# Kernel tuning notes

Measured on AMD Instinct MI355X. Metric: run time of the kernel, lower is better.

Reference implementation:

```python
import jax, jax.numpy as jnp
import numpy as np

HEADS = 16
EPS = 1e-5

def _ln(x, g, b):
    m = jnp.mean(x, axis=-1, keepdims=True)
    v = jnp.mean((x - m) ** 2, axis=-1, keepdims=True)
    return (x - m) * jax.lax.rsqrt(v + EPS) * g + b

def setup_inputs() -> dict:
    key = jax.random.key(0)
    ks = jax.random.split(key, 12)
    B, N, C, H = 4, 2048, 1024, 4096
    d = {}
    d['x'] = jax.random.normal(ks[0], (B, N, C), jnp.float32)
    d['pos_embed'] = jax.random.normal(ks[1], (1, N, C), jnp.float32)
    # LayerNorm params (normq, normk, normv, norm)
    for nm in ['nq', 'nk', 'nv', 'n']:
        d[nm + '_g'] = jnp.ones((C,), jnp.float32)
        d[nm + '_b'] = jnp.zeros((C,), jnp.float32)
    s = 1.0 / np.sqrt(C)
    d['wq'] = jax.random.uniform(ks[2], (C, C), jnp.float32, -s, s)
    d['bq'] = jnp.zeros((C,), jnp.float32)
    d['wk'] = jax.random.uniform(ks[3], (C, C), jnp.float32, -s, s)
    d['bk'] = jnp.zeros((C,), jnp.float32)
    d['wv'] = jax.random.uniform(ks[4], (C, C), jnp.float32, -s, s)
    d['bv'] = jnp.zeros((C,), jnp.float32)
    d['wp'] = jax.random.uniform(ks[5], (C, C), jnp.float32, -s, s)
    d['bp'] = jnp.zeros((C,), jnp.float32)
    d['w1'] = jax.random.uniform(ks[6], (C, H), jnp.float32, -s, s)
    d['b1'] = jnp.zeros((H,), jnp.float32)
    sh = 1.0 / np.sqrt(H)
    d['w2'] = jax.random.uniform(ks[7], (H, C), jnp.float32, -sh, sh)
    d['b2'] = jnp.zeros((C,), jnp.float32)
    return d

def reference(x, pos_embed, nq_g, nq_b, nk_g, nk_b, nv_g, nv_b, wq, bq, wk, bk, wv, bv, wp, bp, n_g, n_b, w1, b1, w2, b2):
    B, N, C = x.shape
    hd = C // HEADS
    scale = hd ** -0.5
    q_in = x
    k_in = x + pos_embed
    v_in = x + pos_embed
    # Attention (eval mode: dropout = identity)
    q = (_ln(q_in, nq_g, nq_b) @ wq + bq).reshape(B, N, HEADS, hd)
    k = (_ln(k_in, nk_g, nk_b) @ wk + bk).reshape(B, N, HEADS, hd)
    v = (_ln(v_in, nv_g, nv_b) @ wv + bv).reshape(B, N, HEADS, hd)
    attn = jnp.einsum('bqhd,bkhd->bhqk', q, k) * scale
    attn = jax.nn.softmax(attn, axis=-1)
    out = jnp.einsum('bhqk,bkhd->bqhd', attn, v).reshape(B, N, C)
    out = out @ wp + bp
    # residual + MLP
    h = q_in + out
    y = _ln(h, n_g, n_b) @ w1 + b1
    y = jnp.where(y >= 0, y, 0.1 * y)  # LeakyReLU(0.1)
    y = y @ w2 + b2
    return h + y
```

## Files before the change

### kernel.cpp

```cpp
#include <hip/hip_runtime.h>
#include <hip/hip_bf16.h>

#define DEV __device__ __forceinline__

typedef __attribute__((ext_vector_type(8))) short short8;
typedef __attribute__((ext_vector_type(4))) short short4v;
typedef __attribute__((ext_vector_type(4))) float f32x4;
typedef __attribute__((ext_vector_type(2))) int int2v;

constexpr int Bb   = 4;
constexpr int SEQ  = 2048;
constexpr int C    = 1024;
constexpr int HID  = 4096;
constexpr int NH   = 16;
constexpr int HD   = 64;
constexpr int MTOT = Bb * SEQ;

DEV unsigned bfbits(float f) {
  unsigned x = __float_as_uint(f);
  return (x + 0x7fffu + ((x >> 16) & 1u)) >> 16;
}

DEV short f2bf(float f) { return (short)bfbits(f); }

DEV unsigned packrn(float a, float b) {
  unsigned ua = __float_as_uint(a) + 0x8000u;
  unsigned ub = __float_as_uint(b) + 0x8000u;
  return __builtin_amdgcn_perm(ub, ua, 0x07060302u);
}

DEV float fexp2(float x) {
#if __has_builtin(__builtin_amdgcn_exp2f)
  return __builtin_amdgcn_exp2f(x);
#else
  float r;
  asm("v_exp_f32 %0, %1" : "=v"(r) : "v"(x));
  return r;
#endif
}

DEV void gload16(const void* g, void* l) {
  __builtin_amdgcn_global_load_lds((const __attribute__((address_space(1))) void*)g,
                                   (__attribute__((address_space(3))) void*)l, 16, 0, 0);
}

DEV f32x4 mfma16(short4v a, short4v b, f32x4 c) {
#if __has_builtin(__builtin_amdgcn_mfma_f32_16x16x16bf16_1k)
  return __builtin_amdgcn_mfma_f32_16x16x16bf16_1k(a, b, c, 0, 0, 0);
#else
  asm volatile("v_mfma_f32_16x16x16_bf16 %0, %1, %2, %0" : "+v"(c) : "v"(a), "v"(b));
  return c;
#endif
}

DEV void transpose_body(const float* __restrict__ src, short* __restrict__ dst,
                        int R, int Cc) {
  __shared__ float t[32][33];
  int tx = threadIdx.x & 31, ty = threadIdx.x >> 5;
  int c0 = blockIdx.x * 32, r0 = blockIdx.y * 32;
  #pragma unroll
  for (int i = 0; i < 4; i++)
    t[ty + i * 8][tx] = src[(size_t)(r0 + ty + i * 8) * Cc + c0 + tx];
  __syncthreads();
  #pragma unroll
  for (int i = 0; i < 4; i++)
    dst[(size_t)(c0 + ty + i * 8) * R + r0 + tx] = f2bf(t[tx][ty + i * 8]);
}

__global__ void k_transpose_w(const float* __restrict__ src, short* __restrict__ dst,
                              int R, int Cc) {
  transpose_body(src, dst, R, Cc);
}

__global__ void k_transpose_w4(const float* __restrict__ s0, const float* __restrict__ s1,
                               const float* __restrict__ s2, const float* __restrict__ s3,
                               short* __restrict__ d0, short* __restrict__ d1,
                               short* __restrict__ d2, short* __restrict__ d3) {
  const float* s = blockIdx.z == 0 ? s0 : blockIdx.z == 1 ? s1 : blockIdx.z == 2 ? s2 : s3;
  short*       d = blockIdx.z == 0 ? d0 : blockIdx.z == 1 ? d1 : blockIdx.z == 2 ? d2 : d3;
  transpose_body(s, d, C, C);
}

__global__ void k_transpose_v(const short* __restrict__ V, short* __restrict__ Vt) {
  __shared__ short t[32][33];
  int tx = threadIdx.x & 31, ty = threadIdx.x >> 5;
  int plane = blockIdx.z;
  int b = plane >> 4, h = plane & 15;
  int n0 = blockIdx.x * 32, d0 = blockIdx.y * 32;
  #pragma unroll
  for (int i = 0; i < 4; i++)
    t[ty + i * 8][tx] = V[(size_t)(b * SEQ + n0 + ty + i * 8) * C + h * HD + d0 + tx];
  __syncthreads();
  #pragma unroll
  for (int i = 0; i < 4; i++)
    Vt[((size_t)plane * HD + d0 + ty + i * 8) * SEQ + n0 + tx] = t[tx][ty + i * 8];
}

__global__ void k_ln_qkv(const float* __restrict__ x, const float* __restrict__ pos,
                         const float* __restrict__ nqg, const float* __restrict__ nqb,
                         const float* __restrict__ nkg, const float* __restrict__ nkb,
                         const float* __restrict__ nvg, const float* __restrict__ nvb,
                         short* __restrict__ xq, short* __restrict__ xk,
                         short* __restrict__ xv) {
  int row = blockIdx.x, tid = threadIdx.x;
  int n = row & (SEQ - 1);
  float a4[4], p4[4];
  float s1 = 0, s2 = 0, t1 = 0, t2 = 0;
  #pragma unroll
  for (int i = 0; i < 4; i++) {
    int c = tid + i * 256;
    float a = x[(size_t)row * C + c];
    float p = pos[(size_t)n * C + c] + a;
    a4[i] = a; p4[i] = p;
    s1 += a; s2 += a * a; t1 += p; t2 += p * p;
  }
  #pragma unroll
  for (int off = 32; off; off >>= 1) {
    s1 += __shfl_xor(s1, off, 64);
    s2 += __shfl_xor(s2, off, 64);
    t1 += __shfl_xor(t1, off, 64);
    t2 += __shfl_xor(t2, off, 64);
  }
  __shared__ float red[4][4];
  int wave = tid >> 6, lane = tid & 63;
  if (lane == 0) { red[wave][0] = s1; red[wave][1] = s2; red[wave][2] = t1; red[wave][3] = t2; }
  __syncthreads();
  s1 = red[0][0] + red[1][0] + red[2][0] + red[3][0];
  s2 = red[0][1] + red[1][1] + red[2][1] + red[3][1];
  t1 = red[0][2] + red[1][2] + red[2][2] + red[3][2];
  t2 = red[0][3] + red[1][3] + red[2][3] + red[3][3];
  float mq = s1 * (1.f / C), mk = t1 * (1.f / C);
  float rq = rsqrtf(s2 * (1.f / C) - mq * mq + 1e-5f);
  float rk = rsqrtf(t2 * (1.f / C) - mk * mk + 1e-5f);
  #pragma unroll
  for (int i = 0; i < 4; i++) {
    int c = tid + i * 256;
    float nq_ = (a4[i] - mq) * rq;
    float nk_ = (p4[i] - mk) * rk;
    xq[(size_t)row * C + c] = f2bf(nq_ * nqg[c] + nqb[c]);
    xk[(size_t)row * C + c] = f2bf(nk_ * nkg[c] + nkb[c]);
    xv[(size_t)row * C + c] = f2bf(nk_ * nvg[c] + nvb[c]);
  }
}

__global__ void k_ln1(const float* __restrict__ h, const float* __restrict__ g,
                      const float* __restrict__ bta, short* __restrict__ out) {
  int row = blockIdx.x, tid = threadIdx.x;
  float a4[4];
  float s1 = 0, s2 = 0;
  #pragma unroll
  for (int i = 0; i < 4; i++) {
    int c = tid + i * 256;
    float a = h[(size_t)row * C + c];
    a4[i] = a; s1 += a; s2 += a * a;
  }
  #pragma unroll
  for (int off = 32; off; off >>= 1) {
    s1 += __shfl_xor(s1, off, 64);
    s2 += __shfl_xor(s2, off, 64);
  }
  __shared__ float red[4][2];
  int wave = tid >> 6, lane = tid & 63;
  if (lane == 0) { red[wave][0] = s1; red[wave][1] = s2; }
  __syncthreads();
  s1 = red[0][0] + red[1][0] + red[2][0] + red[3][0];
  s2 = red[0][1] + red[1][1] + red[2][1] + red[3][1];
  float m = s1 * (1.f / C);
  float r = rsqrtf(s2 * (1.f / C) - m * m + 1e-5f);
  #pragma unroll
  for (int i = 0; i < 4; i++) {
    int c = tid + i * 256;
    out[(size_t)row * C + c] = f2bf((a4[i] - m) * r * g[c] + bta[c]);
  }
}

template <int MODE>
DEV void gemm8_body(const short* __restrict__ A, const short* __restrict__ Bt,
                    const float* __restrict__ bias, const float* __restrict__ resid,
                    void* __restrict__ outp, int Nn, int Kk, float scale,
                    int m0, int n0, short* __restrict__ sA, short* __restrict__ sB) {
  constexpr int AO = 128 * 64, BO = 256 * 64;
  const int tid = threadIdx.x;
  const int wave = tid >> 6, lane = tid & 63, quad = lane >> 4, l15 = lane & 15;
  const int wm = (wave >> 2) * 64, wn = (wave & 3) * 64;

  const int sr = tid >> 3, su = tid & 7;
  const int sx = (su ^ (sr & 7)) * 8;
  const short* gA0 = A + (size_t)(m0 + sr) * Kk + sx;
  const short* gA1 = gA0 + (size_t)64 * Kk;
  const short* gB0 = Bt + (size_t)(n0 + sr) * Kk + sx;
  const short* gB1 = gB0 + (size_t)64 * Kk;
  const short* gB2 = gB0 + (size_t)128 * Kk;
  const short* gB3 = gB0 + (size_t)192 * Kk;

  const f32x4 fzero = {0.f, 0.f, 0.f, 0.f};
  f32x4 acc[4][4];
  #pragma unroll
  for (int mi = 0; mi < 4; mi++)
    #pragma unroll
    for (int ni = 0; ni < 4; ni++) acc[mi][ni] = fzero;

  const int nkt = Kk >> 6;

  auto stg = [&](int t) {
    const int b_ = t % 3, ko = t << 6;
    gload16(gA0 + ko, &sA[(size_t)b_ * AO + (size_t)tid * 8]);
    gload16(gA1 + ko, &sA[(size_t)b_ * AO + (size_t)(512 + tid) * 8]);
    gload16(gB0 + ko, &sB[(size_t)b_ * BO + (size_t)tid * 8]);
    gload16(gB1 + ko, &sB[(size_t)b_ * BO + (size_t)(512 + tid) * 8]);
    gload16(gB2 + ko, &sB[(size_t)b_ * BO + (size_t)(1024 + tid) * 8]);
    gload16(gB3 + ko, &sB[(size_t)b_ * BO + (size_t)(1536 + tid) * 8]);
  };
  auto stgA_ = [&](int t) {
    const int b_ = t % 3, ko = t << 6;
    gload16(gA0 + ko, &sA[(size_t)b_ * AO + (size_t)tid * 8]);
    gload16(gA1 + ko, &sA[(size_t)b_ * AO + (size_t)(512 + tid) * 8]);
    gload16(gB0 + ko, &sB[(size_t)b_ * BO + (size_t)tid * 8]);
  };
  auto stgB_ = [&](int t) {
    const int b_ = t % 3, ko = t << 6;
    gload16(gB1 + ko, &sB[(size_t)b_ * BO + (size_t)(512 + tid) * 8]);
    gload16(gB2 + ko, &sB[(size_t)b_ * BO + (size_t)(1024 + tid) * 8]);
    gload16(gB3 + ko, &sB[(size_t)b_ * BO + (size_t)(1536 + tid) * 8]);
  };

  stg(0);
  if (nkt > 1) stg(1);

  for (int t = 0; t < nkt; t++) {
    if (t + 1 < nkt) asm volatile("s_waitcnt vmcnt(6)" ::: "memory");
    else             asm volatile("s_waitcnt vmcnt(0)" ::: "memory");
    __builtin_amdgcn_s_barrier();
    const short* a_ = &sA[(size_t)(t % 3) * AO];
    const short* b_ = &sB[(size_t)(t % 3) * BO];
    short8 av[4][2];
    {
      short8 bv[2][2];
      #pragma unroll
      for (int m2 = 0; m2 < 4; m2++) {
        const int rA = wm + m2 * 16 + l15, sw = rA & 7;
        #pragma unroll
        for (int ks = 0; ks < 2; ks++)
          av[m2][ks] = *(const short8*)&a_[rA * 64 + ((ks * 4 + quad) ^ sw) * 8];
      }
      #pragma unroll
      for (int n2 = 0; n2 < 2; n2++) {
        const int rB = wn + n2 * 16 + l15, sw = rB & 7;
        #pragma unroll
        for (int ks = 0; ks < 2; ks++)
          bv[n2][ks] = *(const short8*)&b_[rB * 64 + ((ks * 4 + quad) ^ sw) * 8];
      }
      if (t + 2 < nkt) stgA_(t + 2);
      __builtin_amdgcn_s_barrier();
      asm volatile("s_waitcnt lgkmcnt(0)" ::: "memory");
      __builtin_amdgcn_sched_barrier(0);
      __builtin_amdgcn_s_setprio(1);
      #pragma unroll
      for (int ks = 0; ks < 2; ks++)
        #pragma unroll
        for (int m2 = 0; m2 < 4; m2++)
          #pragma unroll
          for (int n2 = 0; n2 < 2; n2++)
            acc[m2][n2] = __builtin_amdgcn_mfma_f32_16x16x32_bf16(
                av[m2][ks], bv[n2][ks], acc[m2][n2], 0, 0, 0);
      __builtin_amdgcn_s_setprio(0);
      __builtin_amdgcn_s_barrier();
    }
    {
      short8 bv[2][2];
      #pragma unroll
      for (int n2 = 0; n2 < 2; n2++) {
        const int rB = wn + (2 + n2) * 16 + l15, sw = rB & 7;
        #pragma unroll
        for (int ks = 0; ks < 2; ks++)
          bv[n2][ks] = *(const short8*)&b_[rB * 64 + ((ks * 4 + quad) ^ sw) * 8];
      }
      if (t + 2 < nkt) stgB_(t + 2);
      __builtin_amdgcn_s_barrier();
      asm volatile("s_waitcnt lgkmcnt(0)" ::: "memory");
      __builtin_amdgcn_sched_barrier(0);
      __builtin_amdgcn_s_setprio(1);
      #pragma unroll
      for (int ks = 0; ks < 2; ks++)
        #pragma unroll
        for (int m2 = 0; m2 < 4; m2++)
          #pragma unroll
          for (int n2 = 0; n2 < 2; n2++)
            acc[m2][2 + n2] = __builtin_amdgcn_mfma_f32_16x16x32_bf16(
                av[m2][ks], bv[n2][ks], acc[m2][2 + n2], 0, 0, 0);
      __builtin_amdgcn_s_setprio(0);
      __builtin_amdgcn_s_barrier();
    }
  }

  float bb[4];
  #pragma unroll
  for (int ni = 0; ni < 4; ni++) bb[ni] = bias[n0 + wn + ni * 16 + l15];
  #pragma unroll
  for (int mi = 0; mi < 4; mi++) {
    #pragma unroll
    for (int ni = 0; ni < 4; ni++) {
      #pragma unroll
      for (int r = 0; r < 4; r++) {
        int row = m0 + wm + mi * 16 + quad * 4 + r;
        int col = n0 + wn + ni * 16 + l15;
        float v = (acc[mi][ni][r] + bb[ni]) * scale;
        if constexpr (MODE == 1) v = v >= 0.f ? v : 0.1f * v;
        if constexpr (MODE == 2)
          ((float*)outp)[(size_t)row * Nn + col] = resid[(size_t)row * Nn + col] + v;
        else
          ((short*)outp)[(size_t)row * Nn + col] = f2bf(v);
      }
    }
  }
}

template <int MODE>
__global__ __launch_bounds__(512, 1)
void k_gemm8(const short* __restrict__ A, const short* __restrict__ Bt,
             const float* __restrict__ bias, const float* __restrict__ resid,
             void* __restrict__ outp, int Nn, int Kk) {
  __shared__ __align__(16) short sA[3 * 128 * 64];
  __shared__ __align__(16) short sB[3 * 256 * 64];
  gemm8_body<MODE>(A, Bt, bias, resid, outp, Nn, Kk, 1.0f,
                   blockIdx.x * 128, blockIdx.y * 256, sA, sB);
}

__global__ __launch_bounds__(512, 1)
void k_gemm8_qkv(const short* __restrict__ xq, const short* __restrict__ xk,
                 const short* __restrict__ xv,
                 const short* __restrict__ wqT, const short* __restrict__ wkT,
                 const short* __restrict__ wvT,
                 const float* __restrict__ bq, const float* __restrict__ bk,
                 const float* __restrict__ bv,
                 short* __restrict__ Qm, short* __restrict__ Km, short* __restrict__ Vm) {
  __shared__ __align__(16) short sA[3 * 128 * 64];
  __shared__ __align__(16) short sB[3 * 256 * 64];
  const int z = blockIdx.z;
  const short* A    = z == 0 ? xq : z == 1 ? xk : xv;
  const short* Bt   = z == 0 ? wqT : z == 1 ? wkT : wvT;
  const float* bias = z == 0 ? bq : z == 1 ? bk : bv;
  short* outp       = z == 0 ? Qm : z == 1 ? Km : Vm;
  const float scale = z == 0 ? 0.1803368801111244f : 1.0f;
  gemm8_body<0>(A, Bt, bias, nullptr, outp, C, C, scale,
                blockIdx.x * 128, blockIdx.y * 256, sA, sB);
}

__global__ __launch_bounds__(256, 4)
void k_attn(const short* __restrict__ Q, const short* __restrict__ K,
            const short* __restrict__ Vt, short* __restrict__ O) {
  __shared__ __align__(16) short sK[2][64 * 64];
  __shared__ __align__(16) short sV[2][64 * 64];
  const int tid = threadIdx.x;
  const int bh = blockIdx.x;
  const int b = bh >> 4, h = bh & 15;
  const int q0 = blockIdx.y * 128;
  const int wave = tid >> 6, lane = tid & 63, quad = lane >> 4, l15 = lane & 15;
  const int wm = wave * 32;
  const size_t tokBase = (size_t)b * SEQ;

  short8 qf[2][2];
  #pragma unroll
  for (int qi = 0; qi < 2; qi++)
    #pragma unroll
    for (int hf = 0; hf < 2; hf++)
      qf[qi][hf] = *(const short8*)(Q + (tokBase + q0 + wm + qi * 16 + l15) * C
                                    + h * HD + hf * 32 + quad * 8);

  const int r0 = tid >> 3,        c0s = ((tid & 7) ^ (r0 & 7)) * 8;
  const int r1 = (tid + 256) >> 3, c1s = ((tid & 7) ^ (r1 & 7)) * 8;
  const short* gK0 = K + (tokBase + r0) * C + h * HD + c0s;
  const short* gK1 = K + (tokBase + r1) * C + h * HD + c1s;
  const short* gV0 = Vt + ((size_t)bh * HD + r0) * SEQ + c0s;
  const short* gV1 = Vt + ((size_t)bh * HD + r1) * SEQ + c1s;
  short* lK0 = &sK[0][tid * 8];
  short* lK1 = &sK[0][(tid + 256) * 8];
  short* lV0 = &sV[0][tid * 8];
  short* lV1 = &sV[0][(tid + 256) * 8];
  constexpr int BUFO = 64 * 64;

#define STAGE(bufsel, kb) {                                   \
    int kk = (kb) * 64, bo = (bufsel) * BUFO;                 \
    gload16(gK0 + (size_t)kk * C, lK0 + bo);                  \
    gload16(gK1 + (size_t)kk * C, lK1 + bo);                  \
    gload16(gV0 + kk,             lV0 + bo);                  \
    gload16(gV1 + kk,             lV1 + bo); }

  const f32x4 fzero = {0.f, 0.f, 0.f, 0.f};
  const short4v onesv = {0x3F80, 0x3F80, 0x3F80, 0x3F80};
  f32x4 o[2][4];
  f32x4 oSum[2] = {fzero, fzero};
  #pragma unroll
  for (int qi = 0; qi < 2; qi++)
    #pragma unroll
    for (int di = 0; di < 4; di++) o[qi][di] = fzero;

  const int sw = l15 & 7;

  STAGE(0, 0)

  for (int kb = 0; kb < SEQ / 64; kb++) {
    const int buf = kb & 1;
    __syncthreads();
    if (kb + 1 < SEQ / 64) STAGE(buf ^ 1, kb + 1)

    unsigned pk[4][2][2];
    #pragma unroll
    for (int ki = 0; ki < 4; ki++) {
      const int krow = (ki * 16 + l15) * 64;
      short8 a0 = *(const short8*)&sK[buf][krow + ((0 + quad) ^ sw) * 8];
      short8 a1 = *(const short8*)&sK[buf][krow + ((4 + quad) ^ sw) * 8];
      #pragma unroll
      for (int qi = 0; qi < 2; qi++) {
        f32x4 st = __builtin_amdgcn_mfma_f32_16x16x32_bf16(a0, qf[qi][0], fzero, 0, 0, 0);
        st = __builtin_amdgcn_mfma_f32_16x16x32_bf16(a1, qf[qi][1], st, 0, 0, 0);
        float p0 = fexp2(st[0]), p1 = fexp2(st[1]);
        float p2 = fexp2(st[2]), p3 = fexp2(st[3]);
        pk[ki][qi][0] = packrn(p0, p1);
        pk[ki][qi][1] = packrn(p2, p3);
      }
    }

    #pragma unroll
    for (int ki = 0; ki < 4; ki++) {
      short4v bv[4];
      const int g = ((ki * 2 + (quad >> 1)) ^ sw) * 8 + (quad & 1) * 4;
      #pragma unroll
      for (int di = 0; di < 4; di++)
        bv[di] = *(const short4v*)&sV[buf][(di * 16 + l15) * 64 + g];
      #pragma unroll
      for (int qi = 0; qi < 2; qi++) {
        int2v t; t.x = (int)pk[ki][qi][0]; t.y = (int)pk[ki][qi][1];
        short4v aP = __builtin_bit_cast(short4v, t);
        oSum[qi] = mfma16(aP, onesv, oSum[qi]);
        #pragma unroll
        for (int di = 0; di < 4; di++)
          o[qi][di] = mfma16(aP, bv[di], o[qi][di]);
      }
    }
  }
#undef STAGE

  float linv[2][4];
  #pragma unroll
  for (int qi = 0; qi < 2; qi++)
    #pragma unroll
    for (int r = 0; r < 4; r++)
      linv[qi][r] = 1.0f / oSum[qi][r];

  #pragma unroll
  for (int qi = 0; qi < 2; qi++)
    #pragma unroll
    for (int di = 0; di < 4; di++)
      #pragma unroll
      for (int r = 0; r < 4; r++) {
        int row = q0 + wm + qi * 16 + quad * 4 + r;
        int col = h * HD + di * 16 + l15;
        O[(tokBase + row) * C + col] = f2bf(o[qi][di][r] * linv[qi][r]);
      }
}

extern "C" void kernel_launch(void* const* d_in, const int* in_sizes, int n_in,
                              void* d_out, int out_size, void* d_ws, size_t ws_size,
                              hipStream_t stream) {
  const float* x   = (const float*)d_in[0];
  const float* pos = (const float*)d_in[1];
  const float* nqg = (const float*)d_in[2];
  const float* nqb = (const float*)d_in[3];
  const float* nkg = (const float*)d_in[4];
  const float* nkb = (const float*)d_in[5];
  const float* nvg = (const float*)d_in[6];
  const float* nvb = (const float*)d_in[7];
  const float* ng  = (const float*)d_in[8];
  const float* nb  = (const float*)d_in[9];
  const float* wq  = (const float*)d_in[10];
  const float* bq  = (const float*)d_in[11];
  const float* wk  = (const float*)d_in[12];
  const float* bk  = (const float*)d_in[13];
  const float* wv  = (const float*)d_in[14];
  const float* bv  = (const float*)d_in[15];
  const float* wp  = (const float*)d_in[16];
  const float* bp  = (const float*)d_in[17];
  const float* w1  = (const float*)d_in[18];
  const float* b1  = (const float*)d_in[19];
  const float* w2  = (const float*)d_in[20];
  const float* b2  = (const float*)d_in[21];

  char* ws = (char*)d_ws;
  const size_t MB = 1u << 20;
  short* wqT  = (short*)(ws + 0 * MB);
  short* wkT  = (short*)(ws + 2 * MB);
  short* wvT  = (short*)(ws + 4 * MB);
  short* wpT  = (short*)(ws + 6 * MB);
  short* w1T  = (short*)(ws + 8 * MB);
  short* w2T  = (short*)(ws + 16 * MB);
  short* xq   = (short*)(ws + 24 * MB);
  short* xk   = (short*)(ws + 40 * MB);
  short* xv   = (short*)(ws + 56 * MB);
  short* Qm   = (short*)(ws + 72 * MB);
  short* Km   = (short*)(ws + 88 * MB);
  short* Vm   = (short*)(ws + 104 * MB);
  short* Vt   = (short*)(ws + 120 * MB);
  short* y1   = (short*)(ws + 72 * MB);
  short* Ob   = xk;
  short* hln  = xq;
  float* hbuf = (float*)(ws + 136 * MB);
  (void)ws_size; (void)in_sizes; (void)n_in; (void)out_size;

  dim3 blk(256);
  k_transpose_w4<<<dim3(32, 32, 4), blk, 0, stream>>>(wq, wk, wv, wp, wqT, wkT, wvT, wpT);
  k_transpose_w<<<dim3(128, 32), blk, 0, stream>>>(w1, w1T, C, HID);
  k_transpose_w<<<dim3(32, 128), blk, 0, stream>>>(w2, w2T, HID, C);
  k_ln_qkv<<<dim3(MTOT), blk, 0, stream>>>(x, pos, nqg, nqb, nkg, nkb, nvg, nvb, xq, xk, xv);
  k_gemm8_qkv<<<dim3(MTOT / 128, C / 256, 3), dim3(512), 0, stream>>>(
      xq, xk, xv, wqT, wkT, wvT, bq, bk, bv, Qm, Km, Vm);
  k_transpose_v<<<dim3(SEQ / 32, HD / 32, Bb * NH), blk, 0, stream>>>(Vm, Vt);
  k_attn<<<dim3(Bb * NH, SEQ / 128), blk, 0, stream>>>(Qm, Km, Vt, Ob);
  k_gemm8<2><<<dim3(MTOT / 128, C / 256), dim3(512), 0, stream>>>(Ob, wpT, bp, x, hbuf, C, C);
  k_ln1<<<dim3(MTOT), blk, 0, stream>>>(hbuf, ng, nb, hln);
  k_gemm8<1><<<dim3(MTOT / 128, HID / 256), dim3(512), 0, stream>>>(hln, w1T, b1, nullptr,
                                                                    y1, HID, C);
  k_gemm8<2><<<dim3(MTOT / 128, C / 256), dim3(512), 0, stream>>>(y1, w2T, b2, hbuf,
                                                                  (float*)d_out, C, HID);
}
```

Before: 524.9 us.

## Enlarge GEMM tiles to 256x256 with double-buffered four-phase staging

```diff
diff --git a/kernel.cpp b/kernel.cpp
--- a/kernel.cpp
+++ b/kernel.cpp
@@ -175,82 +175,66 @@
 }
 
 template <int MODE>
-DEV void gemm8_body(const short* __restrict__ A, const short* __restrict__ Bt,
+DEV void gemm2_body(const short* __restrict__ A, const short* __restrict__ Bt,
                     const float* __restrict__ bias, const float* __restrict__ resid,
                     void* __restrict__ outp, int Nn, int Kk, float scale,
                     int m0, int n0, short* __restrict__ sA, short* __restrict__ sB) {
-  constexpr int AO = 128 * 64, BO = 256 * 64;
+  constexpr int TO = 256 * 64;
   const int tid = threadIdx.x;
   const int wave = tid >> 6, lane = tid & 63, quad = lane >> 4, l15 = lane & 15;
-  const int wm = (wave >> 2) * 64, wn = (wave & 3) * 64;
+  const int wm = (wave >> 2) * 128, wn = (wave & 3) * 64;
 
   const int sr = tid >> 3, su = tid & 7;
   const int sx = (su ^ (sr & 7)) * 8;
   const short* gA0 = A + (size_t)(m0 + sr) * Kk + sx;
-  const short* gA1 = gA0 + (size_t)64 * Kk;
   const short* gB0 = Bt + (size_t)(n0 + sr) * Kk + sx;
-  const short* gB1 = gB0 + (size_t)64 * Kk;
-  const short* gB2 = gB0 + (size_t)128 * Kk;
-  const short* gB3 = gB0 + (size_t)192 * Kk;
 
   const f32x4 fzero = {0.f, 0.f, 0.f, 0.f};
-  f32x4 acc[4][4];
-  #pragma unroll
-  for (int mi = 0; mi < 4; mi++)
+  f32x4 acc[8][4];
+  #pragma unroll
+  for (int mi = 0; mi < 8; mi++)
     #pragma unroll
     for (int ni = 0; ni < 4; ni++) acc[mi][ni] = fzero;
 
   const int nkt = Kk >> 6;
 
-  auto stg = [&](int t) {
-    const int b_ = t % 3, ko = t << 6;
-    gload16(gA0 + ko, &sA[(size_t)b_ * AO + (size_t)tid * 8]);
-    gload16(gA1 + ko, &sA[(size_t)b_ * AO + (size_t)(512 + tid) * 8]);
-    gload16(gB0 + ko, &sB[(size_t)b_ * BO + (size_t)tid * 8]);
-    gload16(gB1 + ko, &sB[(size_t)b_ * BO + (size_t)(512 + tid) * 8]);
-    gload16(gB2 + ko, &sB[(size_t)b_ * BO + (size_t)(1024 + tid) * 8]);
-    gload16(gB3 + ko, &sB[(size_t)b_ * BO + (size_t)(1536 + tid) * 8]);
+  auto stgPair = [&](int t, int p) {
+    const int b_ = t & 1, ko = t << 6;
+    gload16(gA0 + (size_t)(p * 64) * Kk + ko,
+            &sA[(size_t)b_ * TO + (size_t)p * 4096 + (size_t)tid * 8]);
+    gload16(gB0 + (size_t)(p * 64) * Kk + ko,
+            &sB[(size_t)b_ * TO + (size_t)p * 4096 + (size_t)tid * 8]);
   };
-  auto stgA_ = [&](int t) {
-    const int b_ = t % 3, ko = t << 6;
-    gload16(gA0 + ko, &sA[(size_t)b_ * AO + (size_t)tid * 8]);
-    gload16(gA1 + ko, &sA[(size_t)b_ * AO + (size_t)(512 + tid) * 8]);
-    gload16(gB0 + ko, &sB[(size_t)b_ * BO + (size_t)tid * 8]);
-  };
-  auto stgB_ = [&](int t) {
-    const int b_ = t % 3, ko = t << 6;
-    gload16(gB1 + ko, &sB[(size_t)b_ * BO + (size_t)(512 + tid) * 8]);
-    gload16(gB2 + ko, &sB[(size_t)b_ * BO + (size_t)(1024 + tid) * 8]);
-    gload16(gB3 + ko, &sB[(size_t)b_ * BO + (size_t)(1536 + tid) * 8]);
-  };
-
-  stg(0);
-  if (nkt > 1) stg(1);
+
+  #pragma unroll
+  for (int p = 0; p < 4; p++) stgPair(0, p);
 
   for (int t = 0; t < nkt; t++) {
-    if (t + 1 < nkt) asm volatile("s_waitcnt vmcnt(6)" ::: "memory");
-    else             asm volatile("s_waitcnt vmcnt(0)" ::: "memory");
+    asm volatile("s_waitcnt vmcnt(0)" ::: "memory");
     __builtin_amdgcn_s_barrier();
-    const short* a_ = &sA[(size_t)(t % 3) * AO];
-    const short* b_ = &sB[(size_t)(t % 3) * BO];
-    short8 av[4][2];
-    {
-      short8 bv[2][2];
-      #pragma unroll
-      for (int m2 = 0; m2 < 4; m2++) {
-        const int rA = wm + m2 * 16 + l15, sw = rA & 7;
+    const short* a_ = &sA[(size_t)(t & 1) * TO];
+    const short* b_ = &sB[(size_t)(t & 1) * TO];
+    short8 bv[4][2];
+    #pragma unroll
+    for (int ph = 0; ph < 4; ph++) {
+      short8 av[2][2];
+      #pragma unroll
+      for (int m2 = 0; m2 < 2; m2++) {
+        const int rA = wm + (ph * 2 + m2) * 16 + l15, sw = rA & 7;
         #pragma unroll
         for (int ks = 0; ks < 2; ks++)
           av[m2][ks] = *(const short8*)&a_[rA * 64 + ((ks * 4 + quad) ^ sw) * 8];
       }
-      #pragma unroll
-      for (int n2 = 0; n2 < 2; n2++) {
-        const int rB = wn + n2 * 16 + l15, sw = rB & 7;
+      if (ph == 0) {
         #pragma unroll
-        for (int ks = 0; ks < 2; ks++)
-          bv[n2][ks] = *(const short8*)&b_[rB * 64 + ((ks * 4 + quad) ^ sw) * 8];
-      }
-      if (t + 2 < nkt) stgA_(t + 2);
+        for (int n2 = 0; n2 < 4; n2++) {
+          const int rB = wn + n2 * 16 + l15, sw = rB & 7;
+          #pragma unroll
+          for (int ks = 0; ks < 2; ks++)
+            bv[n2][ks] = *(const short8*)&b_[rB * 64 + ((ks * 4 + quad) ^ sw) * 8];
+        }
+      }
+      if (t + 1 < nkt) stgPair(t + 1, ph);
       __builtin_amdgcn_s_barrier();
       asm volatile("s_waitcnt lgkmcnt(0)" ::: "memory");
       __builtin_amdgcn_sched_barrier(0);
@@ -258,46 +242,21 @@
       #pragma unroll
       for (int ks = 0; ks < 2; ks++)
         #pragma unroll
-        for (int m2 = 0; m2 < 4; m2++)
+        for (int m2 = 0; m2 < 2; m2++)
           #pragma unroll
-          for (int n2 = 0; n2 < 2; n2++)
-            acc[m2][n2] = __builtin_amdgcn_mfma_f32_16x16x32_bf16(
-                av[m2][ks], bv[n2][ks], acc[m2][n2], 0, 0, 0);
+          for (int n2 = 0; n2 < 4; n2++)
+            acc[ph * 2 + m2][n2] = __builtin_amdgcn_mfma_f32_16x16x32_bf16(
+                av[m2][ks], bv[n2][ks], acc[ph * 2 + m2][n2], 0, 0, 0);
       __builtin_amdgcn_s_setprio(0);
       __builtin_amdgcn_s_barrier();
     }
-    {
-      short8 bv[2][2];
-      #pragma unroll
-      for (int n2 = 0; n2 < 2; n2++) {
-        const int rB = wn + (2 + n2) * 16 + l15, sw = rB & 7;
-        #pragma unroll
-        for (int ks = 0; ks < 2; ks++)
-          bv[n2][ks] = *(const short8*)&b_[rB * 64 + ((ks * 4 + quad) ^ sw) * 8];
-      }
-      if (t + 2 < nkt) stgB_(t + 2);
-      __builtin_amdgcn_s_barrier();
-      asm volatile("s_waitcnt lgkmcnt(0)" ::: "memory");
-      __builtin_amdgcn_sched_barrier(0);
-      __builtin_amdgcn_s_setprio(1);
-      #pragma unroll
-      for (int ks = 0; ks < 2; ks++)
-        #pragma unroll
-        for (int m2 = 0; m2 < 4; m2++)
-          #pragma unroll
-          for (int n2 = 0; n2 < 2; n2++)
-            acc[m2][2 + n2] = __builtin_amdgcn_mfma_f32_16x16x32_bf16(
-                av[m2][ks], bv[n2][ks], acc[m2][2 + n2], 0, 0, 0);
-      __builtin_amdgcn_s_setprio(0);
-      __builtin_amdgcn_s_barrier();
-    }
   }
 
   float bb[4];
   #pragma unroll
   for (int ni = 0; ni < 4; ni++) bb[ni] = bias[n0 + wn + ni * 16 + l15];
   #pragma unroll
-  for (int mi = 0; mi < 4; mi++) {
+  for (int mi = 0; mi < 8; mi++) {
     #pragma unroll
     for (int ni = 0; ni < 4; ni++) {
       #pragma unroll
@@ -317,33 +276,33 @@
 
 template <int MODE>
 __global__ __launch_bounds__(512, 1)
-void k_gemm8(const short* __restrict__ A, const short* __restrict__ Bt,
+void k_gemm2(const short* __restrict__ A, const short* __restrict__ Bt,
              const float* __restrict__ bias, const float* __restrict__ resid,
              void* __restrict__ outp, int Nn, int Kk) {
-  __shared__ __align__(16) short sA[3 * 128 * 64];
-  __shared__ __align__(16) short sB[3 * 256 * 64];
-  gemm8_body<MODE>(A, Bt, bias, resid, outp, Nn, Kk, 1.0f,
-                   blockIdx.x * 128, blockIdx.y * 256, sA, sB);
+  __shared__ __align__(16) short sA[2 * 256 * 64];
+  __shared__ __align__(16) short sB[2 * 256 * 64];
+  gemm2_body<MODE>(A, Bt, bias, resid, outp, Nn, Kk, 1.0f,
+                   blockIdx.x * 256, blockIdx.y * 256, sA, sB);
 }
 
 __global__ __launch_bounds__(512, 1)
-void k_gemm8_qkv(const short* __restrict__ xq, const short* __restrict__ xk,
+void k_gemm2_qkv(const short* __restrict__ xq, const short* __restrict__ xk,
                  const short* __restrict__ xv,
                  const short* __restrict__ wqT, const short* __restrict__ wkT,
                  const short* __restrict__ wvT,
                  const float* __restrict__ bq, const float* __restrict__ bk,
                  const float* __restrict__ bv,
                  short* __restrict__ Qm, short* __restrict__ Km, short* __restrict__ Vm) {
-  __shared__ __align__(16) short sA[3 * 128 * 64];
-  __shared__ __align__(16) short sB[3 * 256 * 64];
+  __shared__ __align__(16) short sA[2 * 256 * 64];
+  __shared__ __align__(16) short sB[2 * 256 * 64];
   const int z = blockIdx.z;
   const short* A    = z == 0 ? xq : z == 1 ? xk : xv;
   const short* Bt   = z == 0 ? wqT : z == 1 ? wkT : wvT;
   const float* bias = z == 0 ? bq : z == 1 ? bk : bv;
   short* outp       = z == 0 ? Qm : z == 1 ? Km : Vm;
   const float scale = z == 0 ? 0.1803368801111244f : 1.0f;
-  gemm8_body<0>(A, Bt, bias, nullptr, outp, C, C, scale,
-                blockIdx.x * 128, blockIdx.y * 256, sA, sB);
+  gemm2_body<0>(A, Bt, bias, nullptr, outp, C, C, scale,
+                blockIdx.x * 256, blockIdx.y * 256, sA, sB);
 }
 
 __global__ __launch_bounds__(256, 4)
@@ -512,14 +471,14 @@
   k_transpose_w<<<dim3(128, 32), blk, 0, stream>>>(w1, w1T, C, HID);
   k_transpose_w<<<dim3(32, 128), blk, 0, stream>>>(w2, w2T, HID, C);
   k_ln_qkv<<<dim3(MTOT), blk, 0, stream>>>(x, pos, nqg, nqb, nkg, nkb, nvg, nvb, xq, xk, xv);
-  k_gemm8_qkv<<<dim3(MTOT / 128, C / 256, 3), dim3(512), 0, stream>>>(
+  k_gemm2_qkv<<<dim3(MTOT / 256, C / 256, 3), dim3(512), 0, stream>>>(
       xq, xk, xv, wqT, wkT, wvT, bq, bk, bv, Qm, Km, Vm);
   k_transpose_v<<<dim3(SEQ / 32, HD / 32, Bb * NH), blk, 0, stream>>>(Vm, Vt);
   k_attn<<<dim3(Bb * NH, SEQ / 128), blk, 0, stream>>>(Qm, Km, Vt, Ob);
-  k_gemm8<2><<<dim3(MTOT / 128, C / 256), dim3(512), 0, stream>>>(Ob, wpT, bp, x, hbuf, C, C);
+  k_gemm2<2><<<dim3(MTOT / 256, C / 256), dim3(512), 0, stream>>>(Ob, wpT, bp, x, hbuf, C, C);
   k_ln1<<<dim3(MTOT), blk, 0, stream>>>(hbuf, ng, nb, hln);
-  k_gemm8<1><<<dim3(MTOT / 128, HID / 256), dim3(512), 0, stream>>>(hln, w1T, b1, nullptr,
+  k_gemm2<1><<<dim3(MTOT / 256, HID / 256), dim3(512), 0, stream>>>(hln, w1T, b1, nullptr,
                                                                     y1, HID, C);
-  k_gemm8<2><<<dim3(MTOT / 128, C / 256), dim3(512), 0, stream>>>(y1, w2T, b2, hbuf,
+  k_gemm2<2><<<dim3(MTOT / 256, C / 256), dim3(512), 0, stream>>>(y1, w2T, b2, hbuf,
                                                                   (float*)d_out, C, HID);
 }
```

Result: slower. 569.3 us (+8.5%).

## Add 256x256 double-buffered GEMM kernel for QKV and MLP-up projections

Applied to the files above, without the earlier changes.

```diff
diff --git a/kernel.cpp b/kernel.cpp
--- a/kernel.cpp
+++ b/kernel.cpp
@@ -326,24 +326,135 @@
                    blockIdx.x * 128, blockIdx.y * 256, sA, sB);
 }
 
+template <int MODE>
+DEV void gemm2_body(const short* __restrict__ A, const short* __restrict__ Bt,
+                    const float* __restrict__ bias, const float* __restrict__ resid,
+                    void* __restrict__ outp, int Nn, int Kk, float scale,
+                    int m0, int n0, short* __restrict__ sA, short* __restrict__ sB) {
+  constexpr int TO = 256 * 64;
+  const int tid = threadIdx.x;
+  const int wave = tid >> 6, lane = tid & 63, quad = lane >> 4, l15 = lane & 15;
+  const int wm = (wave >> 2) * 128, wn = (wave & 3) * 64;
+
+  const int sr = tid >> 3, su = tid & 7;
+  const int sx = (su ^ (sr & 7)) * 8;
+  const short* gA0 = A + (size_t)(m0 + sr) * Kk + sx;
+  const short* gB0 = Bt + (size_t)(n0 + sr) * Kk + sx;
+
+  const f32x4 fzero = {0.f, 0.f, 0.f, 0.f};
+  f32x4 acc[8][4];
+  #pragma unroll
+  for (int mi = 0; mi < 8; mi++)
+    #pragma unroll
+    for (int ni = 0; ni < 4; ni++) acc[mi][ni] = fzero;
+
+  const int nkt = Kk >> 6;
+
+  auto stgPair = [&](int t, int p) {
+    const int b_ = t & 1, ko = t << 6;
+    gload16(gA0 + (size_t)(p * 64) * Kk + ko,
+            &sA[(size_t)b_ * TO + (size_t)p * 4096 + (size_t)tid * 8]);
+    gload16(gB0 + (size_t)(p * 64) * Kk + ko,
+            &sB[(size_t)b_ * TO + (size_t)p * 4096 + (size_t)tid * 8]);
+  };
+
+  #pragma unroll
+  for (int p = 0; p < 4; p++) stgPair(0, p);
+
+  for (int t = 0; t < nkt; t++) {
+    asm volatile("s_waitcnt vmcnt(0)" ::: "memory");
+    __builtin_amdgcn_s_barrier();
+    const short* a_ = &sA[(size_t)(t & 1) * TO];
+    const short* b_ = &sB[(size_t)(t & 1) * TO];
+    short8 bv[4][2];
+    #pragma unroll
+    for (int ph = 0; ph < 4; ph++) {
+      short8 av[2][2];
+      #pragma unroll
+      for (int m2 = 0; m2 < 2; m2++) {
+        const int rA = wm + (ph * 2 + m2) * 16 + l15, sw = rA & 7;
+        #pragma unroll
+        for (int ks = 0; ks < 2; ks++)
+          av[m2][ks] = *(const short8*)&a_[rA * 64 + ((ks * 4 + quad) ^ sw) * 8];
+      }
+      if (ph == 0) {
+        #pragma unroll
+        for (int n2 = 0; n2 < 4; n2++) {
+          const int rB = wn + n2 * 16 + l15, sw = rB & 7;
+          #pragma unroll
+          for (int ks = 0; ks < 2; ks++)
+            bv[n2][ks] = *(const short8*)&b_[rB * 64 + ((ks * 4 + quad) ^ sw) * 8];
+        }
+      }
+      if (t + 1 < nkt) stgPair(t + 1, ph);
+      __builtin_amdgcn_s_barrier();
+      asm volatile("s_waitcnt lgkmcnt(0)" ::: "memory");
+      __builtin_amdgcn_sched_barrier(0);
+      __builtin_amdgcn_s_setprio(1);
+      #pragma unroll
+      for (int ks = 0; ks < 2; ks++)
+        #pragma unroll
+        for (int m2 = 0; m2 < 2; m2++)
+          #pragma unroll
+          for (int n2 = 0; n2 < 4; n2++)
+            acc[ph * 2 + m2][n2] = __builtin_amdgcn_mfma_f32_16x16x32_bf16(
+                av[m2][ks], bv[n2][ks], acc[ph * 2 + m2][n2], 0, 0, 0);
+      __builtin_amdgcn_s_setprio(0);
+      __builtin_amdgcn_s_barrier();
+    }
+  }
+
+  float bb[4];
+  #pragma unroll
+  for (int ni = 0; ni < 4; ni++) bb[ni] = bias[n0 + wn + ni * 16 + l15];
+  #pragma unroll
+  for (int mi = 0; mi < 8; mi++) {
+    #pragma unroll
+    for (int ni = 0; ni < 4; ni++) {
+      #pragma unroll
+      for (int r = 0; r < 4; r++) {
+        int row = m0 + wm + mi * 16 + quad * 4 + r;
+        int col = n0 + wn + ni * 16 + l15;
+        float v = (acc[mi][ni][r] + bb[ni]) * scale;
+        if constexpr (MODE == 1) v = v >= 0.f ? v : 0.1f * v;
+        if constexpr (MODE == 2)
+          ((float*)outp)[(size_t)row * Nn + col] = resid[(size_t)row * Nn + col] + v;
+        else
+          ((short*)outp)[(size_t)row * Nn + col] = f2bf(v);
+      }
+    }
+  }
+}
+
+template <int MODE>
 __global__ __launch_bounds__(512, 1)
-void k_gemm8_qkv(const short* __restrict__ xq, const short* __restrict__ xk,
+void k_gemm2(const short* __restrict__ A, const short* __restrict__ Bt,
+             const float* __restrict__ bias, const float* __restrict__ resid,
+             void* __restrict__ outp, int Nn, int Kk) {
+  __shared__ __align__(16) short sA[2 * 256 * 64];
+  __shared__ __align__(16) short sB[2 * 256 * 64];
+  gemm2_body<MODE>(A, Bt, bias, resid, outp, Nn, Kk, 1.0f,
+                   blockIdx.x * 256, blockIdx.y * 256, sA, sB);
+}
+
+__global__ __launch_bounds__(512, 1)
+void k_gemm2_qkv(const short* __restrict__ xq, const short* __restrict__ xk,
                  const short* __restrict__ xv,
                  const short* __restrict__ wqT, const short* __restrict__ wkT,
                  const short* __restrict__ wvT,
                  const float* __restrict__ bq, const float* __restrict__ bk,
                  const float* __restrict__ bv,
                  short* __restrict__ Qm, short* __restrict__ Km, short* __restrict__ Vm) {
-  __shared__ __align__(16) short sA[3 * 128 * 64];
-  __shared__ __align__(16) short sB[3 * 256 * 64];
+  __shared__ __align__(16) short sA[2 * 256 * 64];
+  __shared__ __align__(16) short sB[2 * 256 * 64];
   const int z = blockIdx.z;
   const short* A    = z == 0 ? xq : z == 1 ? xk : xv;
   const short* Bt   = z == 0 ? wqT : z == 1 ? wkT : wvT;
   const float* bias = z == 0 ? bq : z == 1 ? bk : bv;
   short* outp       = z == 0 ? Qm : z == 1 ? Km : Vm;
   const float scale = z == 0 ? 0.1803368801111244f : 1.0f;
-  gemm8_body<0>(A, Bt, bias, nullptr, outp, C, C, scale,
-                blockIdx.x * 128, blockIdx.y * 256, sA, sB);
+  gemm2_body<0>(A, Bt, bias, nullptr, outp, C, C, scale,
+                blockIdx.x * 256, blockIdx.y * 256, sA, sB);
 }
 
 __global__ __launch_bounds__(256, 4)
@@ -512,13 +623,13 @@
   k_transpose_w<<<dim3(128, 32), blk, 0, stream>>>(w1, w1T, C, HID);
   k_transpose_w<<<dim3(32, 128), blk, 0, stream>>>(w2, w2T, HID, C);
   k_ln_qkv<<<dim3(MTOT), blk, 0, stream>>>(x, pos, nqg, nqb, nkg, nkb, nvg, nvb, xq, xk, xv);
-  k_gemm8_qkv<<<dim3(MTOT / 128, C / 256, 3), dim3(512), 0, stream>>>(
+  k_gemm2_qkv<<<dim3(MTOT / 256, C / 256, 3), dim3(512), 0, stream>>>(
       xq, xk, xv, wqT, wkT, wvT, bq, bk, bv, Qm, Km, Vm);
   k_transpose_v<<<dim3(SEQ / 32, HD / 32, Bb * NH), blk, 0, stream>>>(Vm, Vt);
   k_attn<<<dim3(Bb * NH, SEQ / 128), blk, 0, stream>>>(Qm, Km, Vt, Ob);
   k_gemm8<2><<<dim3(MTOT / 128, C / 256), dim3(512), 0, stream>>>(Ob, wpT, bp, x, hbuf, C, C);
   k_ln1<<<dim3(MTOT), blk, 0, stream>>>(hbuf, ng, nb, hln);
-  k_gemm8<1><<<dim3(MTOT / 128, HID / 256), dim3(512), 0, stream>>>(hln, w1T, b1, nullptr,
+  k_gemm2<1><<<dim3(MTOT / 256, HID / 256), dim3(512), 0, stream>>>(hln, w1T, b1, nullptr,
                                                                     y1, HID, C);
   k_gemm8<2><<<dim3(MTOT / 128, C / 256), dim3(512), 0, stream>>>(y1, w2T, b2, hbuf,
                                                                   (float*)d_out, C, HID);
```

Result: no change. 518.7 us, median of 2 (-1.2%).
